# Kernel tuning notes

Measured on AMD Instinct MI355X. Metric: run time of the kernel, lower is better.

## Reference

```python
import jax, jax.numpy as jnp
import numpy as np

EPS = 1e-5


def _rmsnorm(x, eps=EPS):
    return x * jax.lax.rsqrt(jnp.mean(x * x, axis=-1, keepdims=True) + eps)


def _bitlinear(x, w):
    # fla-style BitLinear: RMSNorm (no affine) -> 8-bit activation quant (STE)
    # -> ternary weight quant (STE) -> linear. w is [out, in].
    xn = _rmsnorm(x)
    s = 127.0 / jnp.clip(jnp.max(jnp.abs(xn), axis=-1, keepdims=True), 1e-5, None)
    xq = jnp.clip(jnp.round(xn * s), -128.0, 127.0) / s
    xq = xn + jax.lax.stop_gradient(xq - xn)
    ws = 1.0 / jnp.clip(jnp.mean(jnp.abs(w)), 1e-5, None)
    wq = jnp.clip(jnp.round(w * ws), -1.0, 1.0) / ws
    wq = w + jax.lax.stop_gradient(wq - w)
    return jnp.einsum('bld,od->blo', xq, wq)


def _hgrn_scan(i, f):
    # h_t = f_t * h_{t-1} + i_t along axis=2 (seq), h_0 = 0.
    def combine(a, b):
        fa, ia = a
        fb, ib = b
        return fa * fb, ia * fb + ib
    _, h = jax.lax.associative_scan(combine, (f, i), axis=2)
    return h


def _forward(hidden_states, Wi, Wf, Wg, Wo, g_norm_weight, num_heads=1):
    b, l, d = hidden_states.shape
    i = _bitlinear(hidden_states, Wi)
    f = jax.nn.sigmoid(_bitlinear(hidden_states, Wf))
    i = jax.nn.silu(i) * (1.0 - f)  # swiglu(i, 1-f)
    # [b, l, (h d)] -> [b, h, l, d_head]
    i = i.reshape(b, l, num_heads, -1).transpose(0, 2, 1, 3)
    f = f.reshape(b, l, num_heads, -1).transpose(0, 2, 1, 3)
    h = _hgrn_scan(i, f)
    h = h.transpose(0, 2, 1, 3).reshape(b, l, d)
    # FusedRMSNormSwishGate: rmsnorm(g)*weight * h*sigmoid(h)
    g = _bitlinear(hidden_states, Wg)
    o = _rmsnorm(g) * g_norm_weight * (h * jax.nn.sigmoid(h))
    return _bitlinear(o, Wo)


def setup_inputs() -> dict:
    key = jax.random.key(0)
    ks = jax.random.split(key, 5)
    B, L, D = 4, 2048, 2048
    gain = 2 ** (-2.5) * (6.0 / (2 * D)) ** 0.5  # xavier_uniform with gain 2^-2.5
    def w(k):
        return jax.random.uniform(k, (D, D), jnp.float32, -gain, gain)
    return {
        'hidden_states': jax.random.normal(ks[0], (B, L, D), jnp.float32),
        'Wi': w(ks[1]),
        'Wf': w(ks[2]),
        'Wg': w(ks[3]),
        'Wo': w(ks[4]),
        'g_norm_weight': jnp.ones((D,), jnp.float32),
    }


def reference(hidden_states, Wi, Wf, Wg, Wo, g_norm_weight):
    return _forward(hidden_states, Wi, Wf, Wg, Wo, g_norm_weight)
```

## Files before the change

### kernel.cpp

```cpp
#include <hip/hip_runtime.h>
#include <stdint.h>

#define B_DIM 4
#define L_DIM 2048
#define D_DIM 2048
#define M_DIM 8192
#define K_DIM 2048
#define N_DIM 2048
#define WELEM (D_DIM * D_DIM)
#define CHUNK 32
#define NCH (L_DIM / CHUNK)

typedef int v4i __attribute__((ext_vector_type(4)));
typedef unsigned short bfraw;

#define AS1 __attribute__((address_space(1)))
#define AS3 __attribute__((address_space(3)))

__device__ __forceinline__ void gl_lds16(const void* g, void* l) {
    __builtin_amdgcn_global_load_lds((AS1 void*)g, (AS3 void*)l, 16, 0, 0);
}

__device__ __forceinline__ float sigmoidf_(float x) { return 1.0f / (1.0f + expf(-x)); }

__device__ __forceinline__ float bf2f(bfraw u) {
    union { unsigned int i; float f; } c; c.i = ((unsigned int)u) << 16; return c.f;
}
__device__ __forceinline__ bfraw f2bf(float f) {
    union { float f; unsigned int i; } c; c.f = f;
    unsigned int lsb = (c.i >> 16) & 1;
    c.i += 0x7fffu + lsb;
    return (bfraw)(c.i >> 16);
}

__device__ __forceinline__ void store_out(float* p, float v) { *p = v; }
__device__ __forceinline__ void store_out(bfraw* p, float v) { *p = f2bf(v); }

__device__ __forceinline__ float block_sum256(float v) {
#pragma unroll
    for (int off = 32; off > 0; off >>= 1) v += __shfl_down(v, off);
    __shared__ float sb[4];
    int lane = threadIdx.x & 63, wv = threadIdx.x >> 6;
    __syncthreads();
    if (lane == 0) sb[wv] = v;
    __syncthreads();
    return sb[0] + sb[1] + sb[2] + sb[3];
}

__device__ __forceinline__ void block_sum_max256(float& s, float& m) {
#pragma unroll
    for (int off = 32; off > 0; off >>= 1) {
        s += __shfl_down(s, off);
        m = fmaxf(m, __shfl_down(m, off));
    }
    __shared__ float sb2[8];
    int lane = threadIdx.x & 63, wv = threadIdx.x >> 6;
    __syncthreads();
    if (lane == 0) { sb2[wv] = s; sb2[4 + wv] = m; }
    __syncthreads();
    s = sb2[0] + sb2[1] + sb2[2] + sb2[3];
    m = fmaxf(fmaxf(sb2[4], sb2[5]), fmaxf(sb2[6], sb2[7]));
}

__global__ void wstats1(const float* __restrict__ w0, const float* __restrict__ w1,
                        const float* __restrict__ w2, const float* __restrict__ w3,
                        float* __restrict__ wpart) {
    int w = blockIdx.x >> 7;
    int slice = blockIdx.x & 127;
    const float* W = (w == 0) ? w0 : ((w == 1) ? w1 : ((w == 2) ? w2 : w3));
    const float4* p = (const float4*)(W + (size_t)slice * (WELEM / 128));
    float s = 0.f;
    for (int i = threadIdx.x; i < (WELEM / 128 / 4); i += 256) {
        float4 v = p[i];
        s += fabsf(v.x) + fabsf(v.y) + fabsf(v.z) + fabsf(v.w);
    }
    s = block_sum256(s);
    if (threadIdx.x == 0) wpart[blockIdx.x] = s;
}

__global__ void wstats2(const float* __restrict__ wpart, float* __restrict__ wdeq) {
    int w = threadIdx.x >> 6;
    int lane = threadIdx.x & 63;
    float s = wpart[w * 128 + lane] + wpart[w * 128 + 64 + lane];
#pragma unroll
    for (int off = 32; off > 0; off >>= 1) s += __shfl_down(s, off);
    if (lane == 0) wdeq[w] = fmaxf(s * (1.0f / (float)WELEM), 1e-5f);
}

__global__ void wquant(const float* __restrict__ w0, const float* __restrict__ w1,
                       const float* __restrict__ w2, const float* __restrict__ w3,
                       const float* __restrict__ wdeq, int8_t* __restrict__ wq) {
    size_t idx = (size_t)blockIdx.x * 256 + threadIdx.x;
    int w = (int)(idx >> 20);
    size_t g = idx & ((1u << 20) - 1);
    const float* W = (w == 0) ? w0 : ((w == 1) ? w1 : ((w == 2) ? w2 : w3));
    float inv = 1.0f / wdeq[w];
    float4 v = ((const float4*)W)[g];
    int q0 = (int)rintf(v.x * inv); q0 = q0 < -1 ? -1 : (q0 > 1 ? 1 : q0);
    int q1 = (int)rintf(v.y * inv); q1 = q1 < -1 ? -1 : (q1 > 1 ? 1 : q1);
    int q2 = (int)rintf(v.z * inv); q2 = q2 < -1 ? -1 : (q2 > 1 ? 1 : q2);
    int q3 = (int)rintf(v.w * inv); q3 = q3 < -1 ? -1 : (q3 > 1 ? 1 : q3);
    uint32_t p = (uint32_t)(q0 & 0xff) | ((uint32_t)(q1 & 0xff) << 8) |
                 ((uint32_t)(q2 & 0xff) << 16) | ((uint32_t)(q3 & 0xff) << 24);
    ((uint32_t*)(wq + (size_t)w * WELEM))[g] = p;
}

__global__ void act_quant(const float* __restrict__ x, int8_t* __restrict__ xq,
                          float* __restrict__ adeq) {
    int row = blockIdx.x, tid = threadIdx.x;
    const float4* xr = (const float4*)(x + (size_t)row * D_DIM);
    float4 a = xr[2 * tid], b = xr[2 * tid + 1];
    float v[8] = {a.x, a.y, a.z, a.w, b.x, b.y, b.z, b.w};
    float ss = 0.f, mx = 0.f;
#pragma unroll
    for (int j = 0; j < 8; j++) { ss += v[j] * v[j]; mx = fmaxf(mx, fabsf(v[j])); }
    block_sum_max256(ss, mx);
    float inv = rsqrtf(ss * (1.0f / (float)D_DIM) + 1e-5f);
    float anc = fmaxf(mx * inv, 1e-5f);
    float s = 127.0f / anc;
    if (tid == 0) adeq[row] = anc * (1.0f / 127.0f);
    float sc = inv * s;
    int q[8];
#pragma unroll
    for (int j = 0; j < 8; j++) {
        int t = (int)rintf(v[j] * sc);
        q[j] = t < -128 ? -128 : (t > 127 ? 127 : t);
    }
    uint32_t lo = (uint32_t)(q[0] & 0xff) | ((uint32_t)(q[1] & 0xff) << 8) |
                  ((uint32_t)(q[2] & 0xff) << 16) | ((uint32_t)(q[3] & 0xff) << 24);
    uint32_t hi = (uint32_t)(q[4] & 0xff) | ((uint32_t)(q[5] & 0xff) << 8) |
                  ((uint32_t)(q[6] & 0xff) << 16) | ((uint32_t)(q[7] & 0xff) << 24);
    ((uint2*)(xq + (size_t)row * D_DIM))[tid] = make_uint2(lo, hi);
}

#define BM 128
#define BN 128
#define BKB 128

template <typename OutT>
__global__ __launch_bounds__(256) void gemm_i8(
    const int8_t* __restrict__ A, const int8_t* __restrict__ Bw,
    const float* __restrict__ adeq, const float* __restrict__ wdeq, int widx,
    OutT* __restrict__ Cout) {
    __shared__ int8_t sA[BM * BKB];
    __shared__ int8_t sB[BN * BKB];
    int m0 = blockIdx.y * BM;
    int n0 = blockIdx.x * BN;
    int lane = threadIdx.x & 63;
    int wv = threadIdx.x >> 6;
    int wm = (wv >> 1) * 64;
    int wn = (wv & 1) * 64;

    const v4i vzero = {0, 0, 0, 0};
    v4i acc[4][4];
#pragma unroll
    for (int i = 0; i < 4; i++)
#pragma unroll
        for (int j = 0; j < 4; j++) acc[i][j] = vzero;

    int rS = lane >> 3;
    int cS = (lane & 7) * 16;
    const int8_t* Ablk = A + (size_t)m0 * K_DIM;
    const int8_t* Bblk = Bw + (size_t)n0 * K_DIM;
    int qq = lane >> 4;
    int mr = lane & 15;

    for (int kt = 0; kt < K_DIM; kt += BKB) {
#pragma unroll
        for (int g = 0; g < 4; g++) {
            int rb = wv * 8 + g * 32;
            gl_lds16(Ablk + (size_t)(rb + rS) * K_DIM + kt + cS, sA + rb * BKB);
            gl_lds16(Bblk + (size_t)(rb + rS) * K_DIM + kt + cS, sB + rb * BKB);
        }
        __syncthreads();

#pragma unroll
        for (int kk = 0; kk < 2; kk++) {
            v4i afrag[4], bfrag[4];
#pragma unroll
            for (int i = 0; i < 4; i++)
                afrag[i] = *(const v4i*)(sA + (size_t)(wm + i * 16 + mr) * BKB + kk * 64 + qq * 16);
#pragma unroll
            for (int j = 0; j < 4; j++)
                bfrag[j] = *(const v4i*)(sB + (size_t)(wn + j * 16 + mr) * BKB + kk * 64 + qq * 16);
#pragma unroll
            for (int i = 0; i < 4; i++)
#pragma unroll
                for (int j = 0; j < 4; j++)
                    acc[i][j] = __builtin_amdgcn_mfma_i32_16x16x64_i8(afrag[i], bfrag[j], acc[i][j], 0, 0, 0);
        }
        __syncthreads();
    }

    float wsc = wdeq[widx];
    int cc = lane & 15;
#pragma unroll
    for (int i = 0; i < 4; i++) {
#pragma unroll
        for (int r = 0; r < 4; r++) {
            int row = m0 + wm + i * 16 + qq * 4 + r;
            float rs = adeq[row] * wsc;
            OutT* crow = Cout + (size_t)row * N_DIM + n0 + wn + cc;
#pragma unroll
            for (int j = 0; j < 4; j++) store_out(crow + j * 16, (float)acc[i][j][r] * rs);
        }
    }
}

__global__ void scan1(const bfraw* __restrict__ iL, const bfraw* __restrict__ fL,
                      float* __restrict__ Fc, float* __restrict__ Ic) {
    int idx = blockIdx.x * 256 + threadIdx.x;
    int d = idx & (D_DIM - 1);
    int c = (idx >> 11) & (NCH - 1);
    int b = idx >> 17;
    size_t base = ((size_t)(b * L_DIM + c * CHUNK)) * D_DIM + d;
    float F = 1.f, h = 0.f;
#pragma unroll 4
    for (int t = 0; t < CHUNK; t++) {
        float fr = bf2f(fL[base + (size_t)t * D_DIM]);
        float ir = bf2f(iL[base + (size_t)t * D_DIM]);
        float fv = sigmoidf_(fr);
        float iv = ir * sigmoidf_(ir) * (1.0f - fv);
        h = fv * h + iv;
        F *= fv;
    }
    size_t ci = ((size_t)b * NCH + c) * D_DIM + d;
    Fc[ci] = F;
    Ic[ci] = h;
}

__global__ void scan2(const float* __restrict__ Fc, const float* __restrict__ Ic,
                      float* __restrict__ Hc) {
    int idx = blockIdx.x * 256 + threadIdx.x;
    int d = idx & (D_DIM - 1);
    int b = idx >> 11;
    float h = 0.f;
    for (int c0 = 0; c0 < NCH; c0 += 8) {
        float F[8], I[8];
#pragma unroll
        for (int j = 0; j < 8; j++) {
            size_t ci = ((size_t)b * NCH + c0 + j) * D_DIM + d;
            F[j] = Fc[ci];
            I[j] = Ic[ci];
        }
#pragma unroll
        for (int j = 0; j < 8; j++) {
            size_t ci = ((size_t)b * NCH + c0 + j) * D_DIM + d;
            Hc[ci] = h;
            h = F[j] * h + I[j];
        }
    }
}

__global__ void scan3(const bfraw* __restrict__ iL, const bfraw* __restrict__ fL,
                      const float* __restrict__ Hc, bfraw* __restrict__ hout) {
    int idx = blockIdx.x * 256 + threadIdx.x;
    int d = idx & (D_DIM - 1);
    int c = (idx >> 11) & (NCH - 1);
    int b = idx >> 17;
    size_t base = ((size_t)(b * L_DIM + c * CHUNK)) * D_DIM + d;
    float h = Hc[((size_t)b * NCH + c) * D_DIM + d];
#pragma unroll 4
    for (int t = 0; t < CHUNK; t++) {
        size_t a = base + (size_t)t * D_DIM;
        float fr = bf2f(fL[a]);
        float ir = bf2f(iL[a]);
        float fv = sigmoidf_(fr);
        float iv = ir * sigmoidf_(ir) * (1.0f - fv);
        h = fv * h + iv;
        hout[a] = f2bf(h);
    }
}

union BF8 { uint4 u; bfraw s[8]; };

__global__ void gout_quant(const bfraw* __restrict__ gL, const bfraw* __restrict__ h,
                           const float* __restrict__ gw, int8_t* __restrict__ oq,
                           float* __restrict__ odeq) {
    int row = blockIdx.x, tid = threadIdx.x;
    BF8 g8, h8;
    g8.u = ((const uint4*)(gL + (size_t)row * D_DIM))[tid];
    float gv[8];
    float ss = 0.f;
#pragma unroll
    for (int j = 0; j < 8; j++) { gv[j] = bf2f(g8.s[j]); ss += gv[j] * gv[j]; }
    float ssg = block_sum256(ss);
    float invg = rsqrtf(ssg * (1.0f / (float)D_DIM) + 1e-5f);

    h8.u = ((const uint4*)(h + (size_t)row * D_DIM))[tid];
    const float4* wr = (const float4*)gw;
    float4 w0 = wr[2 * tid], w1 = wr[2 * tid + 1];
    float wv[8] = {w0.x, w0.y, w0.z, w0.w, w1.x, w1.y, w1.z, w1.w};
    float o[8];
    float sso = 0.f, amax = 0.f;
#pragma unroll
    for (int j = 0; j < 8; j++) {
        float hv = bf2f(h8.s[j]);
        o[j] = gv[j] * invg * wv[j] * hv * sigmoidf_(hv);
        sso += o[j] * o[j];
        amax = fmaxf(amax, fabsf(o[j]));
    }
    block_sum_max256(sso, amax);
    float invo = rsqrtf(sso * (1.0f / (float)D_DIM) + 1e-5f);
    float anc = fmaxf(amax * invo, 1e-5f);
    float s = 127.0f / anc;
    if (tid == 0) odeq[row] = anc * (1.0f / 127.0f);
    float sc = invo * s;
    int q[8];
#pragma unroll
    for (int j = 0; j < 8; j++) {
        int t = (int)rintf(o[j] * sc);
        q[j] = t < -128 ? -128 : (t > 127 ? 127 : t);
    }
    uint32_t lo = (uint32_t)(q[0] & 0xff) | ((uint32_t)(q[1] & 0xff) << 8) |
                  ((uint32_t)(q[2] & 0xff) << 16) | ((uint32_t)(q[3] & 0xff) << 24);
    uint32_t hi = (uint32_t)(q[4] & 0xff) | ((uint32_t)(q[5] & 0xff) << 8) |
                  ((uint32_t)(q[6] & 0xff) << 16) | ((uint32_t)(q[7] & 0xff) << 24);
    ((uint2*)(oq + (size_t)row * D_DIM))[tid] = make_uint2(lo, hi);
}

extern "C" void kernel_launch(void* const* d_in, const int* in_sizes, int n_in,
                              void* d_out, int out_size, void* d_ws, size_t ws_size,
                              hipStream_t stream) {
    const float* x  = (const float*)d_in[0];
    const float* Wi = (const float*)d_in[1];
    const float* Wf = (const float*)d_in[2];
    const float* Wg = (const float*)d_in[3];
    const float* Wo = (const float*)d_in[4];
    const float* gw = (const float*)d_in[5];
    float* out = (float*)d_out;

    char* ws = (char*)d_ws;
    float*  wdeq  = (float*)(ws + 0);
    float*  wpart = (float*)(ws + 256);
    float*  adeq  = (float*)(ws + 0x10000);
    float*  odeq  = (float*)(ws + 0x20000);
    int8_t* xq    = (int8_t*)(ws + 0x100000);
    int8_t* wq    = (int8_t*)(ws + 0x1100000);
    float*  Fc    = (float*)(ws + 0x2100000);
    float*  Ic    = (float*)(ws + 0x2300000);
    float*  Hc    = (float*)(ws + 0x2500000);
    bfraw*  bufI  = (bfraw*)(ws + 0x4000000);
    bfraw*  bufF  = (bfraw*)(ws + 0x6000000);
    bfraw*  hbuf  = (bfraw*)(ws + 0x8000000);

    wstats1<<<512, 256, 0, stream>>>(Wi, Wf, Wg, Wo, wpart);
    wstats2<<<1, 256, 0, stream>>>(wpart, wdeq);
    wquant<<<16384, 256, 0, stream>>>(Wi, Wf, Wg, Wo, wdeq, wq);
    act_quant<<<M_DIM, 256, 0, stream>>>(x, xq, adeq);

    dim3 ggrid(N_DIM / BN, M_DIM / BM);
    gemm_i8<bfraw><<<ggrid, 256, 0, stream>>>(xq, wq + 0 * (size_t)WELEM, adeq, wdeq, 0, bufI);
    gemm_i8<bfraw><<<ggrid, 256, 0, stream>>>(xq, wq + 1 * (size_t)WELEM, adeq, wdeq, 1, bufF);

    scan1<<<2048, 256, 0, stream>>>(bufI, bufF, Fc, Ic);
    scan2<<<32, 256, 0, stream>>>(Fc, Ic, Hc);
    scan3<<<2048, 256, 0, stream>>>(bufI, bufF, Hc, hbuf);

    gemm_i8<bfraw><<<ggrid, 256, 0, stream>>>(xq, wq + 2 * (size_t)WELEM, adeq, wdeq, 2, bufI);
    gout_quant<<<M_DIM, 256, 0, stream>>>(bufI, hbuf, gw, xq , odeq);
    gemm_i8<float><<<ggrid, 256, 0, stream>>>(xq , wq + 3 * (size_t)WELEM, odeq, wdeq, 3, out);

    (void)in_sizes; (void)n_in; (void)out_size; (void)ws_size;
}
```

Measured before the change: 493.0 us.

## Batch I/F/G GEMMs into one launch, widen GEMM tile, merge quant kernels

Merges weight and activation quantization into a single kernel launch. The three input projection GEMMs (I, F, G) now run as one grid, with G written to its own buffer so it is no longer recomputed after the scan. The GEMM tile changes to 128x256 with K-step 64, giving 4x8 MFMA accumulators per wave, and launch bounds request 2 blocks per CU. The aim is fewer launches, better wave fill and more reuse per LDS load. The cost is higher register pressure, plus an extra 32MB buffer and a halved K step, which means twice as many barriers.

```diff
diff --git a/kernel.cpp b/kernel.cpp
--- a/kernel.cpp
+++ b/kernel.cpp
@@ -87,27 +87,28 @@
     if (lane == 0) wdeq[w] = fmaxf(s * (1.0f / (float)WELEM), 1e-5f);
 }
 
-__global__ void wquant(const float* __restrict__ w0, const float* __restrict__ w1,
-                       const float* __restrict__ w2, const float* __restrict__ w3,
-                       const float* __restrict__ wdeq, int8_t* __restrict__ wq) {
-    size_t idx = (size_t)blockIdx.x * 256 + threadIdx.x;
-    int w = (int)(idx >> 20);
-    size_t g = idx & ((1u << 20) - 1);
-    const float* W = (w == 0) ? w0 : ((w == 1) ? w1 : ((w == 2) ? w2 : w3));
-    float inv = 1.0f / wdeq[w];
-    float4 v = ((const float4*)W)[g];
-    int q0 = (int)rintf(v.x * inv); q0 = q0 < -1 ? -1 : (q0 > 1 ? 1 : q0);
-    int q1 = (int)rintf(v.y * inv); q1 = q1 < -1 ? -1 : (q1 > 1 ? 1 : q1);
-    int q2 = (int)rintf(v.z * inv); q2 = q2 < -1 ? -1 : (q2 > 1 ? 1 : q2);
-    int q3 = (int)rintf(v.w * inv); q3 = q3 < -1 ? -1 : (q3 > 1 ? 1 : q3);
-    uint32_t p = (uint32_t)(q0 & 0xff) | ((uint32_t)(q1 & 0xff) << 8) |
-                 ((uint32_t)(q2 & 0xff) << 16) | ((uint32_t)(q3 & 0xff) << 24);
-    ((uint32_t*)(wq + (size_t)w * WELEM))[g] = p;
-}
-
-__global__ void act_quant(const float* __restrict__ x, int8_t* __restrict__ xq,
+__global__ void quant_all(const float* __restrict__ w0, const float* __restrict__ w1,
+                          const float* __restrict__ w2, const float* __restrict__ w3,
+                          const float* __restrict__ wdeq, int8_t* __restrict__ wq,
+                          const float* __restrict__ x, int8_t* __restrict__ xq,
                           float* __restrict__ adeq) {
-    int row = blockIdx.x, tid = threadIdx.x;
+    if (blockIdx.x < 16384) {
+        size_t idx = (size_t)blockIdx.x * 256 + threadIdx.x;
+        int w = (int)(idx >> 20);
+        size_t g = idx & ((1u << 20) - 1);
+        const float* W = (w == 0) ? w0 : ((w == 1) ? w1 : ((w == 2) ? w2 : w3));
+        float inv = 1.0f / wdeq[w];
+        float4 v = ((const float4*)W)[g];
+        int q0 = (int)rintf(v.x * inv); q0 = q0 < -1 ? -1 : (q0 > 1 ? 1 : q0);
+        int q1 = (int)rintf(v.y * inv); q1 = q1 < -1 ? -1 : (q1 > 1 ? 1 : q1);
+        int q2 = (int)rintf(v.z * inv); q2 = q2 < -1 ? -1 : (q2 > 1 ? 1 : q2);
+        int q3 = (int)rintf(v.w * inv); q3 = q3 < -1 ? -1 : (q3 > 1 ? 1 : q3);
+        uint32_t p = (uint32_t)(q0 & 0xff) | ((uint32_t)(q1 & 0xff) << 8) |
+                     ((uint32_t)(q2 & 0xff) << 16) | ((uint32_t)(q3 & 0xff) << 24);
+        ((uint32_t*)(wq + (size_t)w * WELEM))[g] = p;
+        return;
+    }
+    int row = blockIdx.x - 16384, tid = threadIdx.x;
     const float4* xr = (const float4*)(x + (size_t)row * D_DIM);
     float4 a = xr[2 * tid], b = xr[2 * tid + 1];
     float v[8] = {a.x, a.y, a.z, a.w, b.x, b.y, b.z, b.w};
@@ -134,65 +135,60 @@
 }
 
 #define BM 128
-#define BN 128
-#define BKB 128
+#define BN 256
+#define BKB 64
 
 template <typename OutT>
-__global__ __launch_bounds__(256) void gemm_i8(
+__device__ __forceinline__ void gemm_core(
     const int8_t* __restrict__ A, const int8_t* __restrict__ Bw,
-    const float* __restrict__ adeq, const float* __restrict__ wdeq, int widx,
-    OutT* __restrict__ Cout) {
+    const float* __restrict__ adeq, float wsc,
+    int m0, int n0, OutT* __restrict__ Cout) {
     __shared__ int8_t sA[BM * BKB];
     __shared__ int8_t sB[BN * BKB];
-    int m0 = blockIdx.y * BM;
-    int n0 = blockIdx.x * BN;
     int lane = threadIdx.x & 63;
     int wv = threadIdx.x >> 6;
-    int wm = (wv >> 1) * 64;
-    int wn = (wv & 1) * 64;
+    int wm = (wv & 1) * 64;
+    int wn = (wv >> 1) * 128;
 
     const v4i vzero = {0, 0, 0, 0};
-    v4i acc[4][4];
+    v4i acc[4][8];
 #pragma unroll
     for (int i = 0; i < 4; i++)
 #pragma unroll
-        for (int j = 0; j < 4; j++) acc[i][j] = vzero;
-
-    int rS = lane >> 3;
-    int cS = (lane & 7) * 16;
+        for (int j = 0; j < 8; j++) acc[i][j] = vzero;
+
+    int rS = lane >> 2;
+    int cS = (lane & 3) * 16;
     const int8_t* Ablk = A + (size_t)m0 * K_DIM;
     const int8_t* Bblk = Bw + (size_t)n0 * K_DIM;
     int qq = lane >> 4;
     int mr = lane & 15;
 
     for (int kt = 0; kt < K_DIM; kt += BKB) {
+        gl_lds16(Ablk + (size_t)(wv * 16 + rS) * K_DIM + kt + cS, sA + (wv * 16) * BKB);
+        gl_lds16(Ablk + (size_t)(64 + wv * 16 + rS) * K_DIM + kt + cS, sA + (64 + wv * 16) * BKB);
 #pragma unroll
         for (int g = 0; g < 4; g++) {
-            int rb = wv * 8 + g * 32;
-            gl_lds16(Ablk + (size_t)(rb + rS) * K_DIM + kt + cS, sA + rb * BKB);
+            int rb = g * 64 + wv * 16;
             gl_lds16(Bblk + (size_t)(rb + rS) * K_DIM + kt + cS, sB + rb * BKB);
         }
         __syncthreads();
 
-#pragma unroll
-        for (int kk = 0; kk < 2; kk++) {
-            v4i afrag[4], bfrag[4];
-#pragma unroll
-            for (int i = 0; i < 4; i++)
-                afrag[i] = *(const v4i*)(sA + (size_t)(wm + i * 16 + mr) * BKB + kk * 64 + qq * 16);
-#pragma unroll
-            for (int j = 0; j < 4; j++)
-                bfrag[j] = *(const v4i*)(sB + (size_t)(wn + j * 16 + mr) * BKB + kk * 64 + qq * 16);
-#pragma unroll
-            for (int i = 0; i < 4; i++)
-#pragma unroll
-                for (int j = 0; j < 4; j++)
-                    acc[i][j] = __builtin_amdgcn_mfma_i32_16x16x64_i8(afrag[i], bfrag[j], acc[i][j], 0, 0, 0);
-        }
+        v4i afrag[4], bfrag[8];
+#pragma unroll
+        for (int i = 0; i < 4; i++)
+            afrag[i] = *(const v4i*)(sA + (size_t)(wm + i * 16 + mr) * BKB + qq * 16);
+#pragma unroll
+        for (int j = 0; j < 8; j++)
+            bfrag[j] = *(const v4i*)(sB + (size_t)(wn + j * 16 + mr) * BKB + qq * 16);
+#pragma unroll
+        for (int i = 0; i < 4; i++)
+#pragma unroll
+            for (int j = 0; j < 8; j++)
+                acc[i][j] = __builtin_amdgcn_mfma_i32_16x16x64_i8(afrag[i], bfrag[j], acc[i][j], 0, 0, 0);
         __syncthreads();
     }
 
-    float wsc = wdeq[widx];
     int cc = lane & 15;
 #pragma unroll
     for (int i = 0; i < 4; i++) {
@@ -202,9 +198,28 @@
             float rs = adeq[row] * wsc;
             OutT* crow = Cout + (size_t)row * N_DIM + n0 + wn + cc;
 #pragma unroll
-            for (int j = 0; j < 4; j++) store_out(crow + j * 16, (float)acc[i][j][r] * rs);
+            for (int j = 0; j < 8; j++) store_out(crow + j * 16, (float)acc[i][j][r] * rs);
         }
     }
+}
+
+__global__ __launch_bounds__(256, 2) void gemm_ifg(
+    const int8_t* __restrict__ xq, const int8_t* __restrict__ wq,
+    const float* __restrict__ adeq, const float* __restrict__ wdeq,
+    bfraw* __restrict__ bufI, bfraw* __restrict__ bufF, bfraw* __restrict__ bufG) {
+    int widx = blockIdx.x >> 3;
+    int n0 = (blockIdx.x & 7) * BN;
+    int m0 = blockIdx.y * BM;
+    bfraw* outp = (widx == 0) ? bufI : ((widx == 1) ? bufF : bufG);
+    gemm_core<bfraw>(xq, wq + (size_t)widx * WELEM, adeq, wdeq[widx], m0, n0, outp);
+}
+
+__global__ __launch_bounds__(256, 2) void gemm_o(
+    const int8_t* __restrict__ oq, const int8_t* __restrict__ wq,
+    const float* __restrict__ odeq, const float* __restrict__ wdeq,
+    float* __restrict__ out) {
+    gemm_core<float>(oq, wq + 3 * (size_t)WELEM, odeq, wdeq[3], blockIdx.y * BM,
+                     blockIdx.x * BN, out);
 }
 
 __global__ void scan1(const bfraw* __restrict__ iL, const bfraw* __restrict__ fL,
@@ -342,24 +357,21 @@
     float*  Hc    = (float*)(ws + 0x2500000);
     bfraw*  bufI  = (bfraw*)(ws + 0x4000000);
     bfraw*  bufF  = (bfraw*)(ws + 0x6000000);
-    bfraw*  hbuf  = (bfraw*)(ws + 0x8000000);
+    bfraw*  bufG  = (bfraw*)(ws + 0x8000000);
+    bfraw*  hbuf  = (bfraw*)(ws + 0xA000000);
 
     wstats1<<<512, 256, 0, stream>>>(Wi, Wf, Wg, Wo, wpart);
     wstats2<<<1, 256, 0, stream>>>(wpart, wdeq);
-    wquant<<<16384, 256, 0, stream>>>(Wi, Wf, Wg, Wo, wdeq, wq);
-    act_quant<<<M_DIM, 256, 0, stream>>>(x, xq, adeq);
-
-    dim3 ggrid(N_DIM / BN, M_DIM / BM);
-    gemm_i8<bfraw><<<ggrid, 256, 0, stream>>>(xq, wq + 0 * (size_t)WELEM, adeq, wdeq, 0, bufI);
-    gemm_i8<bfraw><<<ggrid, 256, 0, stream>>>(xq, wq + 1 * (size_t)WELEM, adeq, wdeq, 1, bufF);
+    quant_all<<<16384 + 8192, 256, 0, stream>>>(Wi, Wf, Wg, Wo, wdeq, wq, x, xq, adeq);
+
+    gemm_ifg<<<dim3(24, M_DIM / BM), 256, 0, stream>>>(xq, wq, adeq, wdeq, bufI, bufF, bufG);
 
     scan1<<<2048, 256, 0, stream>>>(bufI, bufF, Fc, Ic);
     scan2<<<32, 256, 0, stream>>>(Fc, Ic, Hc);
     scan3<<<2048, 256, 0, stream>>>(bufI, bufF, Hc, hbuf);
 
-    gemm_i8<bfraw><<<ggrid, 256, 0, stream>>>(xq, wq + 2 * (size_t)WELEM, adeq, wdeq, 2, bufI);
-    gout_quant<<<M_DIM, 256, 0, stream>>>(bufI, hbuf, gw, xq , odeq);
-    gemm_i8<float><<<ggrid, 256, 0, stream>>>(xq , wq + 3 * (size_t)WELEM, odeq, wdeq, 3, out);
+    gout_quant<<<M_DIM, 256, 0, stream>>>(bufG, hbuf, gw, xq , odeq);
+    gemm_o<<<dim3(N_DIM / BN, M_DIM / BM), 256, 0, stream>>>(xq , wq, odeq, wdeq, out);
 
     (void)in_sizes; (void)n_in; (void)out_size; (void)ws_size;
 }
```

After: 430.9 us. 1.14x faster.
